# Kernel optimization log

Measured on AMD Instinct MI355X. Metric: run time of the kernel, lower is better.

## Reference

```python
import jax, jax.numpy as jnp
import numpy as np

B, T, N, D = 16, 24, 2048, 64
L, K = 2, 3  # num_layers, cheb_k


def setup_inputs() -> dict:
    key = jax.random.key(0)
    ks = jax.random.split(key, 6)
    x = jax.random.normal(ks[0], (B, T, N, D), dtype=jnp.float32)
    init_state = jnp.zeros((L, B, N, D), dtype=jnp.float32)
    adj = jax.random.uniform(ks[1], (N, N), dtype=jnp.float32)
    adj = adj / jnp.sum(adj, axis=-1, keepdims=True)  # row-normalized adjacency
    cin = 2 * D
    Wg = jax.random.normal(ks[2], (L, K, cin, 2 * D), dtype=jnp.float32) * (1.0 / np.sqrt(K * cin))
    bg = jnp.zeros((L, 2 * D), dtype=jnp.float32)
    Wu = jax.random.normal(ks[3], (L, K, cin, D), dtype=jnp.float32) * (1.0 / np.sqrt(K * cin))
    bu = jnp.zeros((L, D), dtype=jnp.float32)
    return {"x": x, "init_state": init_state, "adj_matrix": adj,
            "Wg": Wg, "bg": bg, "Wu": Wu, "bu": bu}


def _cheb_supports(adj, k):
    # T0=I, T1=A, Tk = 2*A@T_{k-1} - T_{k-2}
    n = adj.shape[0]
    sup = [jnp.eye(n, dtype=adj.dtype), adj]
    for _ in range(2, k):
        sup.append(2.0 * adj @ sup[-1] - sup[-2])
    return jnp.stack(sup[:k], axis=0)  # [K, N, N]


def _gconv(xs, supports, W, b):
    # xs: [B,N,Cin], supports: [K,N,N], W: [K,Cin,Cout]
    xg = jnp.einsum('knm,bmc->bknc', supports, xs)
    return jnp.einsum('bknc,kco->bno', xg, W) + b


def _cell(x_t, state, supports, Wg_l, bg_l, Wu_l, bu_l):
    ins = jnp.concatenate([x_t, state], axis=-1)  # [B,N,2D]
    zr = jax.nn.sigmoid(_gconv(ins, supports, Wg_l, bg_l))
    z, r = jnp.split(zr, 2, axis=-1)
    cand_in = jnp.concatenate([x_t, z * state], axis=-1)
    hc = jnp.tanh(_gconv(cand_in, supports, Wu_l, bu_l))
    return r * state + (1.0 - r) * hc


def reference(x, init_state, adj_matrix, Wg, bg, Wu, bu):
    supports = _cheb_supports(adj_matrix, K)
    current = x  # [B,T,N,D]
    hiddens = []
    for l in range(L):
        def step(state, x_t, l=l):
            new = _cell(x_t, state, supports, Wg[l], bg[l], Wu[l], bu[l])
            return new, new
        last, seq = jax.lax.scan(step, init_state[l], jnp.swapaxes(current, 0, 1))
        hiddens.append(last)
        current = x + jnp.swapaxes(seq, 0, 1)  # residual over the stacked states
    return current, jnp.stack(hiddens, axis=0)
```

## Files before the change

### kernel.cpp

```cpp
#include <hip/hip_runtime.h>
#include <hip/hip_bf16.h>
#include <math.h>

typedef __bf16 bf16x8 __attribute__((ext_vector_type(8)));
typedef float f32x4 __attribute__((ext_vector_type(4)));
typedef __hip_bfloat16 bf16s;

constexpr int kB = 16, kT = 24, kN = 2048, kD = 64;
constexpr size_t kBND = (size_t)kB * kN * kD;

struct Slot { const void* p0; const void* p1; int astr0, trow0, astr1, trow1, type; };
struct Slots6 { Slot s[6]; };
struct DiffGrp { const bf16s* src; bf16s* oA; bf16s* oA2; };
struct DiffP { const bf16s* S0; const bf16s* S1; DiffGrp g[4]; int colsPerGrp; };

__device__ __forceinline__ void async_copy16(void* lds, const void* g) {
  __builtin_amdgcn_global_load_lds((const __attribute__((address_space(1))) void*)g,
                                   (__attribute__((address_space(3))) void*)lds,
                                   16, 0, 0);
}


__device__ __forceinline__ void diff_core(
    const bf16s* __restrict__ S, const bf16s* __restrict__ Bsrc,
    int m0, int c0, bf16s* lA, bf16s* lB, f32x4 (&acc)[4][4])
{
  const int tid = threadIdx.x, lane = tid & 63, wave = tid >> 6;
  const int wm = (wave >> 1) * 64, wn = (wave & 1) * 64;
  const f32x4 zero = {0.f, 0.f, 0.f, 0.f};
#pragma unroll
  for (int i = 0; i < 4; ++i)
#pragma unroll
    for (int j = 0; j < 4; ++j) acc[i][j] = zero;

  const int ra = tid >> 3;
  const int cs = ((tid & 7) ^ (ra & 7)) * 8;
  const int rk0 = ((lane >> 4) ^ (lane & 7)) * 8;
  const int rk1 = ((4 + (lane >> 4)) ^ (lane & 7)) * 8;

  for (int k0 = 0; k0 < 2048; k0 += 64) {
#pragma unroll
    for (int i = 0; i < 4; ++i) {
      async_copy16(lA + (size_t)(i * 256 + tid) * 8,
                   S + (size_t)(m0 + i * 32 + ra) * 2048 + k0 + cs);
      async_copy16(lB + (size_t)(i * 256 + tid) * 8,
                   Bsrc + (size_t)(c0 + i * 32 + ra) * 2048 + k0 + cs);
    }
    __syncthreads();
#pragma unroll
    for (int ks = 0; ks < 2; ++ks) {
      const int rk = ks ? rk1 : rk0;
      bf16x8 av[4], bv[4];
#pragma unroll
      for (int f = 0; f < 4; ++f) {
        av[f] = *(const bf16x8*)(lA + (size_t)(wm + f * 16 + (lane & 15)) * 64 + rk);
        bv[f] = *(const bf16x8*)(lB + (size_t)(wn + f * 16 + (lane & 15)) * 64 + rk);
      }
#pragma unroll
      for (int i = 0; i < 4; ++i)
#pragma unroll
        for (int j = 0; j < 4; ++j)
          acc[i][j] = __builtin_amdgcn_mfma_f32_16x16x32_bf16(av[i], bv[j], acc[i][j], 0, 0, 0);
    }
    __syncthreads();
  }
}

__global__ __launch_bounds__(256) void k_diff(DiffP p)
{
  __shared__ bf16s lA[128 * 64];
  __shared__ bf16s lB[128 * 64];
  const int mi = blockIdx.x;
  const bf16s* S = (mi >> 4) ? p.S1 : p.S0;
  const int m0 = (mi & 15) * 128;
  const int ybpg = p.colsPerGrp >> 7;
  const int grp = blockIdx.y / ybpg;
  const int c0 = (blockIdx.y - grp * ybpg) * 128;
  const DiffGrp G = p.g[grp];

  f32x4 acc[4][4];
  diff_core(S, G.src, m0, c0, lA, lB, acc);

  bf16s* out = (mi >> 4) ? G.oA2 : G.oA;
  const int lane = threadIdx.x & 63, wave = threadIdx.x >> 6;
  const int wm = (wave >> 1) * 64, wn = (wave & 1) * 64;
  const int rq = (lane >> 4) * 4, cl = lane & 15;
#pragma unroll
  for (int fm = 0; fm < 4; ++fm)
#pragma unroll
    for (int fn = 0; fn < 4; ++fn)
#pragma unroll
      for (int q = 0; q < 4; ++q) {
        int gm = m0 + wm + fm * 16 + rq + q;
        int gc = c0 + wn + fn * 16 + cl;
        size_t off = ((size_t)(gc >> 6) * 2048 + gm) * 64 + (gc & 63);
        out[off] = __float2bfloat16(acc[fm][fn][q]);
      }
}

__global__ __launch_bounds__(256) void k_a2(
    const bf16s* __restrict__ A, const bf16s* __restrict__ AT, bf16s* A2)
{
  __shared__ bf16s lA[128 * 64];
  __shared__ bf16s lB[128 * 64];
  const int m0 = blockIdx.x * 128, n0 = blockIdx.y * 128;
  f32x4 acc[4][4];
  diff_core(A, AT, m0, n0, lA, lB, acc);
  const int lane = threadIdx.x & 63, wave = threadIdx.x >> 6;
  const int wm = (wave >> 1) * 64, wn = (wave & 1) * 64;
  const int rq = (lane >> 4) * 4, cl = lane & 15;
#pragma unroll
  for (int fm = 0; fm < 4; ++fm)
#pragma unroll
    for (int fn = 0; fn < 4; ++fn)
#pragma unroll
      for (int q = 0; q < 4; ++q) {
        int gm = m0 + wm + fm * 16 + rq + q;
        int gc = n0 + wn + fn * 16 + cl;
        A2[(size_t)gm * 2048 + gc] = __float2bfloat16(2.f * acc[fm][fn][q] - (gm == gc ? 1.f : 0.f));
      }
}

template<int BN>
__device__ __forceinline__ void small_core(
    const Slots6& sl, int m0, const bf16s* __restrict__ W,
    bf16s* lA, bf16s* lB, f32x4 (&acc)[4][BN / 32])
{
  const int tid = threadIdx.x, lane = tid & 63, wave = tid >> 6;
  const int wm = (wave >> 1) * 64, wn = (wave & 1) * (BN / 2);
  const f32x4 zero = {0.f, 0.f, 0.f, 0.f};
#pragma unroll
  for (int i = 0; i < 4; ++i)
#pragma unroll
    for (int j = 0; j < BN / 32; ++j) acc[i][j] = zero;

  const int ra = tid >> 3;
  const int cs = ((tid & 7) ^ (ra & 7)) * 8;
  const int rk0 = ((lane >> 4) ^ (lane & 7)) * 8;
  const int rk1 = ((4 + (lane >> 4)) ^ (lane & 7)) * 8;

#pragma unroll
  for (int ks = 0; ks < 6; ++ks) {
    const Slot sd = sl.s[ks];
    if (sd.type == 0) {
      const bf16s* base = (const bf16s*)sd.p0;
#pragma unroll
      for (int i = 0; i < 4; ++i) {
        int row = m0 + i * 32 + ra;
        size_t roff = ((size_t)(row >> 11) * sd.astr0 + sd.trow0 + (row & 2047)) * 64 + cs;
        async_copy16(lA + (size_t)(i * 256 + tid) * 8, base + roff);
      }
    } else if (sd.type == 1) {
#pragma unroll
      for (int i = 0; i < 4; ++i) {
        int row = m0 + i * 32 + ra;
        size_t roff = ((size_t)(row >> 11) * sd.astr0 + sd.trow0 + (row & 2047)) * 64 + cs;
        const float4* q0 = (const float4*)((const float*)sd.p0 + roff);
        float4 a = q0[0], b = q0[1];
        union { bf16x8 v; bf16s h[8]; } u;
        u.h[0] = __float2bfloat16(a.x); u.h[1] = __float2bfloat16(a.y);
        u.h[2] = __float2bfloat16(a.z); u.h[3] = __float2bfloat16(a.w);
        u.h[4] = __float2bfloat16(b.x); u.h[5] = __float2bfloat16(b.y);
        u.h[6] = __float2bfloat16(b.z); u.h[7] = __float2bfloat16(b.w);
        *(bf16x8*)(lA + (size_t)(i * 256 + tid) * 8) = u.v;
      }
    } else {
#pragma unroll
      for (int i = 0; i < 4; ++i) {
        int row = m0 + i * 32 + ra;
        size_t r0o = ((size_t)(row >> 11) * sd.astr0 + sd.trow0 + (row & 2047)) * 64 + cs;
        size_t r1o = ((size_t)(row >> 11) * sd.astr1 + sd.trow1 + (row & 2047)) * 64 + cs;
        union { bf16x8 v; bf16s h[8]; } a, b, o;
        a.v = *(const bf16x8*)((const bf16s*)sd.p0 + r0o);
        b.v = *(const bf16x8*)((const bf16s*)sd.p1 + r1o);
#pragma unroll
        for (int j = 0; j < 8; ++j)
          o.h[j] = __float2bfloat16(__bfloat162float(a.h[j]) + __bfloat162float(b.h[j]));
        *(bf16x8*)(lA + (size_t)(i * 256 + tid) * 8) = o.v;
      }
    }
#pragma unroll
    for (int i = 0; i < BN / 32; ++i)
      async_copy16(lB + (size_t)(i * 256 + tid) * 8,
                   W + (size_t)(i * 32 + ra) * 384 + ks * 64 + cs);
    __syncthreads();
#pragma unroll
    for (int kss = 0; kss < 2; ++kss) {
      const int rk = kss ? rk1 : rk0;
      bf16x8 av[4], bv[BN / 32];
#pragma unroll
      for (int f = 0; f < 4; ++f)
        av[f] = *(const bf16x8*)(lA + (size_t)(wm + f * 16 + (lane & 15)) * 64 + rk);
#pragma unroll
      for (int f = 0; f < BN / 32; ++f)
        bv[f] = *(const bf16x8*)(lB + (size_t)(wn + f * 16 + (lane & 15)) * 64 + rk);
#pragma unroll
      for (int i = 0; i < 4; ++i)
#pragma unroll
        for (int j = 0; j < BN / 32; ++j)
          acc[i][j] = __builtin_amdgcn_mfma_f32_16x16x32_bf16(av[i], bv[j], acc[i][j], 0, 0, 0);
    }
    __syncthreads();
  }
}

struct LayerG {
  Slots6 sl; const bf16s* W; const float* bias;
  const float* h; bf16s* zh; bf16s* zhT; float* r;
};
__global__ __launch_bounds__(256) void k_gate(LayerG A, LayerG B, int nA)
{
  __shared__ bf16s lA[128 * 64];
  __shared__ bf16s lB[128 * 64];
  const int bx = blockIdx.x;
  const bool isA = bx < nA;
  const LayerG L = isA ? A : B;
  const int m0 = (isA ? bx : bx - nA) * 128;
  f32x4 acc[4][4];
  small_core<128>(L.sl, m0, L.W, lA, lB, acc);
  const int lane = threadIdx.x & 63, wave = threadIdx.x >> 6;
  const int wm = (wave >> 1) * 64, wn = (wave & 1) * 64;
  const int rq = (lane >> 4) * 4, cl = lane & 15;
#pragma unroll
  for (int fm = 0; fm < 4; ++fm)
#pragma unroll
    for (int fn = 0; fn < 4; ++fn) {
      const int o = wn + fn * 16 + cl;
      const float bias = L.bias[o];
#pragma unroll
      for (int q = 0; q < 4; ++q) {
        size_t gm = (size_t)m0 + wm + fm * 16 + rq + q;
        float s = 1.f / (1.f + expf(-(acc[fm][fn][q] + bias)));
        if (o < 64) {
          float zh = s * L.h[gm * 64 + o];
          L.zh[gm * 64 + o] = __float2bfloat16(zh);
          L.zhT[((size_t)((gm >> 11) * 64 + o)) * 2048 + (gm & 2047)] = __float2bfloat16(zh);
        } else {
          L.r[gm * 64 + (o - 64)] = s;
        }
      }
    }
}

struct LayerC {
  Slots6 sl; const bf16s* W; const float* bias;
  const float* r; float* h32; bf16s* hT; bf16s* h_bf; float* hid;
  bf16s* x1;
  float* outC;
  const float* x0; int t;
};
__global__ __launch_bounds__(256) void k_cand(LayerC A, LayerC B, int nA)
{
  __shared__ bf16s lA[128 * 64];
  __shared__ bf16s lB[64 * 64];
  const int bx = blockIdx.x;
  const bool isA = bx < nA;
  const LayerC L = isA ? A : B;
  const int m0 = (isA ? bx : bx - nA) * 128;
  f32x4 acc[4][2];
  small_core<64>(L.sl, m0, L.W, lA, lB, acc);
  const int lane = threadIdx.x & 63, wave = threadIdx.x >> 6;
  const int wm = (wave >> 1) * 64, wn = (wave & 1) * 32;
  const int rq = (lane >> 4) * 4, cl = lane & 15;
#pragma unroll
  for (int fm = 0; fm < 4; ++fm)
#pragma unroll
    for (int fn = 0; fn < 2; ++fn) {
      const int d = wn + fn * 16 + cl;
      const float bias = L.bias[d];
#pragma unroll
      for (int q = 0; q < 4; ++q) {
        size_t gm = (size_t)m0 + wm + fm * 16 + rq + q;
        float hc = tanhf(acc[fm][fn][q] + bias);
        float r = L.r[gm * 64 + d];
        float h = L.h32[gm * 64 + d];
        float hn = r * h + (1.f - r) * hc;
        L.h32[gm * 64 + d] = hn;
        int b = (int)(gm >> 11), n = (int)(gm & 2047);
        L.hT[((size_t)(b * 64 + d)) * 2048 + n] = __float2bfloat16(hn);
        L.h_bf[gm * 64 + d] = __float2bfloat16(hn);
        size_t xi = (((size_t)b * kT + L.t) * 2048 + n) * 64 + d;
        if (L.x1) L.x1[gm * 64 + d] = __float2bfloat16(L.x0[xi] + hn);
        if (L.outC) L.outC[xi] = L.x0[xi] + hn;
        if (L.hid) L.hid[gm * 64 + d] = hn;
      }
    }
}

__global__ __launch_bounds__(256) void transpose_cvt(
    const float* in, bf16s* out, int nrows, int ncols,
    size_t in_ostride, size_t out_ostride)
{
  __shared__ float tile[64][65];
  const int r0 = blockIdx.x * 64, c0 = blockIdx.y * 64;
  in  += (size_t)blockIdx.z * in_ostride;
  out += (size_t)blockIdx.z * out_ostride;
  const int tx = threadIdx.x & 63, ty = threadIdx.x >> 6;
#pragma unroll
  for (int i = 0; i < 64; i += 4)
    tile[ty + i][tx] = in[(size_t)(r0 + ty + i) * ncols + c0 + tx];
  __syncthreads();
#pragma unroll
  for (int i = 0; i < 64; i += 4)
    out[(size_t)(c0 + ty + i) * nrows + r0 + tx] = __float2bfloat16(tile[tx][ty + i]);
}

__global__ __launch_bounds__(256) void k_cvt(const float* in, bf16s* out, int n)
{
  int i = blockIdx.x * 256 + threadIdx.x;
  if (i < n) out[i] = __float2bfloat16(in[i]);
}

__global__ __launch_bounds__(256) void k_repack(
    const float* Wg, const float* Wu, bf16s* WgT, bf16s* WuT)
{
  int idx = blockIdx.x * 256 + threadIdx.x;
  if (idx < 2 * 3 * 128 * 128) {
    int o = idx & 127, cin = (idx >> 7) & 127, k = (idx >> 14) % 3, l = idx / 49152;
    WgT[((size_t)(l * 128 + o)) * 384 + (2 * k + (cin >> 6)) * 64 + (cin & 63)] =
        __float2bfloat16(Wg[idx]);
  }
  if (idx < 2 * 3 * 128 * 64) {
    int o = idx & 63, cin = (idx >> 6) & 127, k = (idx >> 13) % 3, l = idx / 24576;
    WuT[((size_t)(l * 64 + o)) * 384 + (2 * k + (cin >> 6)) * 64 + (cin & 63)] =
        __float2bfloat16(Wu[idx]);
  }
}

__global__ __launch_bounds__(256) void init_layer(
    const float* ist_l, float* h32, bf16s* hT, bf16s* h_bf)
{
  size_t idx = (size_t)blockIdx.x * 256 + threadIdx.x;
  if (idx >= kBND) return;
  int d = (int)(idx & 63);
  size_t row = idx >> 6;
  int n = (int)(row & 2047), b = (int)(row >> 11);
  float h = ist_l[idx];
  h32[idx] = h;
  hT[((size_t)(b * 64 + d)) * 2048 + n] = __float2bfloat16(h);
  h_bf[idx] = __float2bfloat16(h);
}

extern "C" void kernel_launch(void* const* d_in, const int* in_sizes, int n_in,
                              void* d_out, int out_size, void* d_ws, size_t ws_size,
                              hipStream_t stream)
{
  (void)in_sizes; (void)n_in; (void)out_size; (void)ws_size;
  const float* x   = (const float*)d_in[0];
  const float* ist = (const float*)d_in[1];
  const float* adj = (const float*)d_in[2];
  const float* Wg  = (const float*)d_in[3];
  const float* bg  = (const float*)d_in[4];
  const float* Wu  = (const float*)d_in[5];
  const float* bu  = (const float*)d_in[6];
  float* outCur = (float*)d_out;
  float* outHid = outCur + (size_t)kB * kT * kN * kD;

  char* p = (char*)d_ws;
  auto carve = [&](size_t bytes) { char* q = p; p += (bytes + 255) & ~(size_t)255; return q; };
  bf16s* A_bf  = (bf16s*)carve((size_t)2048 * 2048 * 2);
  bf16s* A2_bf = (bf16s*)carve((size_t)2048 * 2048 * 2);
  bf16s* WgT   = (bf16s*)carve((size_t)2 * 128 * 384 * 2);
  bf16s* WuT   = (bf16s*)carve((size_t)2 * 64 * 384 * 2);
  float* h32b  = (float*)carve(2 * kBND * 4);
  float* r32b  = (float*)carve(2 * kBND * 4);
  bf16s* hTb   = (bf16s*)carve(2 * kBND * 2);
  bf16s* hbfb  = (bf16s*)carve(2 * kBND * 2);
  bf16s* zhTb  = (bf16s*)carve(2 * kBND * 2);
  bf16s* zhbfb = (bf16s*)carve(2 * kBND * 2);
  bf16s* x1b   = (bf16s*)carve(2 * kBND * 2);
  bf16s* sAh0  = (bf16s*)carve(kBND * 2);
  bf16s* sA2h0 = (bf16s*)carve(kBND * 2);
  bf16s* sAh1  = (bf16s*)carve(kBND * 2);
  bf16s* sA2h1 = (bf16s*)carve(kBND * 2);
  bf16s* sZ0   = (bf16s*)carve(kBND * 2);
  bf16s* sA2Z0 = (bf16s*)carve(kBND * 2);
  bf16s* sZ1   = (bf16s*)carve(kBND * 2);
  bf16s* sA2Z1 = (bf16s*)carve(kBND * 2);
  const size_t xTfull = (size_t)kB * kT * kD * kN * 2;
  bf16s* AxF  = (bf16s*)carve(xTfull);
  bf16s* A2xF = (bf16s*)carve(xTfull);
  bf16s* xTh  = (bf16s*)carve(xTfull / 2);
  bf16s* AT_bf = AxF;

  float* h32_0 = h32b;   float* h32_1 = h32b + kBND;
  float* r32_0 = r32b;   float* r32_1 = r32b + kBND;
  bf16s* hT0 = hTb;      bf16s* hT1 = hTb + kBND;
  bf16s* hbf0 = hbfb;    bf16s* hbf1 = hbfb + kBND;
  bf16s* zhT0 = zhTb;    bf16s* zhT1 = zhTb + kBND;
  bf16s* zhbf0 = zhbfb;  bf16s* zhbf1 = zhbfb + kBND;

  k_cvt<<<dim3((2048 * 2048 + 255) / 256), 256, 0, stream>>>(adj, A_bf, 2048 * 2048);
  transpose_cvt<<<dim3(32, 32, 1), 256, 0, stream>>>(adj, AT_bf, 2048, 2048, 0, 0);
  k_a2<<<dim3(16, 16, 1), 256, 0, stream>>>(A_bf, AT_bf, A2_bf);
  k_repack<<<dim3(384), 256, 0, stream>>>(Wg, Wu, WgT, WuT);
  init_layer<<<dim3((int)(kBND / 256)), 256, 0, stream>>>(ist, h32_0, hT0, hbf0);
  init_layer<<<dim3((int)(kBND / 256)), 256, 0, stream>>>(ist + kBND, h32_1, hT1, hbf1);

  for (int h = 0; h < 2; ++h) {
    size_t off = (size_t)h * 8 * kT * 131072;
    transpose_cvt<<<dim3(32, 1, 8 * kT), 256, 0, stream>>>(x + off, xTh, 2048, 64, 131072, 131072);
    DiffP dp; dp.S0 = A_bf; dp.S1 = A2_bf; dp.colsPerGrp = 12288;
    dp.g[0] = DiffGrp{xTh, AxF + off, A2xF + off};
    dp.g[1] = dp.g[2] = dp.g[3] = DiffGrp{nullptr, nullptr, nullptr};
    k_diff<<<dim3(32, 96), 256, 0, stream>>>(dp);
  }

  auto Sb = [](const void* p0, int astr, int trow) {
    return Slot{p0, nullptr, astr, trow, 0, 0, 0};
  };
  auto Sf = [](const void* p0, int astr, int trow) {
    return Slot{p0, nullptr, astr, trow, 0, 0, 1};
  };
  auto S2 = [](const void* p0, const void* p1, int astr1, int trow1) {
    return Slot{p0, p1, 2048, 0, astr1, trow1, 2};
  };

  for (int s = 0; s <= kT; ++s) {
    const bool aA = (s < kT), aB = (s >= 1);
    const int tA = s, tB = s - 1;
    const int nA = aA ? 256 : 0, nB = aB ? 256 : 0;
    bf16s* x1cur = x1b + (size_t)(s & 1) * kBND;
    bf16s* x1prev = x1b + (size_t)((s - 1) & 1) * kBND;

    {
      DiffP dp; dp.S0 = A_bf; dp.S1 = A2_bf; dp.colsPerGrp = 1024;
      int ng = 0;
      dp.g[ng++] = DiffGrp{hT0, sAh0, sA2h0};
      if (aB) dp.g[ng++] = DiffGrp{hT1, sAh1, sA2h1};
      for (int i = ng; i < 4; ++i) dp.g[i] = DiffGrp{nullptr, nullptr, nullptr};
      k_diff<<<dim3(32, 8 * ng), 256, 0, stream>>>(dp);
    }

    {
      LayerG GA = {}, GB = {};
      if (aA) {
        GA.sl.s[0] = Sf(x, kT * 2048, tA * 2048);
        GA.sl.s[1] = Sb(hbf0, 2048, 0);
        GA.sl.s[2] = Sb(AxF, kT * 2048, tA * 2048);
        GA.sl.s[3] = Sb(sAh0, 2048, 0);
        GA.sl.s[4] = Sb(A2xF, kT * 2048, tA * 2048);
        GA.sl.s[5] = Sb(sA2h0, 2048, 0);
        GA.W = WgT; GA.bias = bg; GA.h = h32_0; GA.zh = zhbf0; GA.zhT = zhT0; GA.r = r32_0;
      }
      if (aB) {
        GB.sl.s[0] = Sb(x1prev, 2048, 0);
        GB.sl.s[1] = Sb(hbf1, 2048, 0);
        GB.sl.s[2] = S2(sAh0, AxF, kT * 2048, tB * 2048);
        GB.sl.s[3] = Sb(sAh1, 2048, 0);
        GB.sl.s[4] = S2(sA2h0, A2xF, kT * 2048, tB * 2048);
        GB.sl.s[5] = Sb(sA2h1, 2048, 0);
        GB.W = WgT + (size_t)128 * 384; GB.bias = bg + 128;
        GB.h = h32_1; GB.zh = zhbf1; GB.zhT = zhT1; GB.r = r32_1;
      }
      k_gate<<<dim3(nA + nB), 256, 0, stream>>>(GA, GB, nA);
    }

    {
      DiffP dp; dp.S0 = A_bf; dp.S1 = A2_bf; dp.colsPerGrp = 1024;
      int ng = 0;
      if (aA) dp.g[ng++] = DiffGrp{zhT0, sZ0, sA2Z0};
      if (aB) dp.g[ng++] = DiffGrp{zhT1, sZ1, sA2Z1};
      for (int i = ng; i < 4; ++i) dp.g[i] = DiffGrp{nullptr, nullptr, nullptr};
      k_diff<<<dim3(32, 8 * ng), 256, 0, stream>>>(dp);
    }

    {
      LayerC CA = {}, CB = {};
      if (aA) {
        CA.sl.s[0] = Sf(x, kT * 2048, tA * 2048);
        CA.sl.s[1] = Sb(zhbf0, 2048, 0);
        CA.sl.s[2] = Sb(AxF, kT * 2048, tA * 2048);
        CA.sl.s[3] = Sb(sZ0, 2048, 0);
        CA.sl.s[4] = Sb(A2xF, kT * 2048, tA * 2048);
        CA.sl.s[5] = Sb(sA2Z0, 2048, 0);
        CA.W = WuT; CA.bias = bu; CA.r = r32_0; CA.h32 = h32_0; CA.hT = hT0; CA.h_bf = hbf0;
        CA.hid = (tA == kT - 1) ? outHid : nullptr;
        CA.x1 = x1cur; CA.outC = nullptr; CA.x0 = x; CA.t = tA;
      }
      if (aB) {
        CB.sl.s[0] = Sb(x1prev, 2048, 0);
        CB.sl.s[1] = Sb(zhbf1, 2048, 0);
        CB.sl.s[2] = S2(sAh0, AxF, kT * 2048, tB * 2048);
        CB.sl.s[3] = Sb(sZ1, 2048, 0);
        CB.sl.s[4] = S2(sA2h0, A2xF, kT * 2048, tB * 2048);
        CB.sl.s[5] = Sb(sA2Z1, 2048, 0);
        CB.W = WuT + (size_t)64 * 384; CB.bias = bu + 64;
        CB.r = r32_1; CB.h32 = h32_1; CB.hT = hT1; CB.h_bf = hbf1;
        CB.hid = (tB == kT - 1) ? outHid + kBND : nullptr;
        CB.x1 = nullptr; CB.outC = outCur; CB.x0 = x; CB.t = tB;
      }
      k_cand<<<dim3(nA + nB), 256, 0, stream>>>(CA, CB, nA);
    }
  }
}
```

Baseline: 5.091 ms.

## Fuse candidate-path diffusion of z*h into the candidate GEMM kernel

Replaces the separate k_diff launch for z*h and the k_cand launch with a single k_dcand kernel. Each block first computes A@zh and A2@zh for a 64-node by two-batch tile, sharing the zh tile between both supports. It writes the results to global memory, then runs the candidate GEMM and GRU update on exactly those rows. This removes one launch and one kernel boundary per timestep and improves locality of the diffusion outputs. In exchange, the diffusion and GEMM phases within a block run serially, and the kernel always launches 512 blocks, with inactive layers exiting early.

```diff
diff --git a/kernel.cpp b/kernel.cpp
--- a/kernel.cpp
+++ b/kernel.cpp
@@ -64,6 +64,28 @@
     }
     __syncthreads();
   }
+}
+
+__device__ __forceinline__ void diff_tile(
+    const bf16s* __restrict__ S, const bf16s* __restrict__ src, bf16s* out,
+    int m0, int c0, bf16s* lA, bf16s* lB)
+{
+  f32x4 acc[4][4];
+  diff_core(S, src, m0, c0, lA, lB, acc);
+  const int lane = threadIdx.x & 63, wave = threadIdx.x >> 6;
+  const int wm = (wave >> 1) * 64, wn = (wave & 1) * 64;
+  const int rq = (lane >> 4) * 4, cl = lane & 15;
+#pragma unroll
+  for (int fm = 0; fm < 4; ++fm)
+#pragma unroll
+    for (int fn = 0; fn < 4; ++fn)
+#pragma unroll
+      for (int q = 0; q < 4; ++q) {
+        int gm = m0 + wm + fm * 16 + rq + q;
+        int gc = c0 + wn + fn * 16 + cl;
+        size_t off = ((size_t)(gc >> 6) * 2048 + gm) * 64 + (gc & 63);
+        out[off] = __float2bfloat16(acc[fm][fn][q]);
+      }
 }
 
 __global__ __launch_bounds__(256) void k_diff(DiffP p)
@@ -77,25 +99,8 @@
   const int grp = blockIdx.y / ybpg;
   const int c0 = (blockIdx.y - grp * ybpg) * 128;
   const DiffGrp G = p.g[grp];
-
-  f32x4 acc[4][4];
-  diff_core(S, G.src, m0, c0, lA, lB, acc);
-
   bf16s* out = (mi >> 4) ? G.oA2 : G.oA;
-  const int lane = threadIdx.x & 63, wave = threadIdx.x >> 6;
-  const int wm = (wave >> 1) * 64, wn = (wave & 1) * 64;
-  const int rq = (lane >> 4) * 4, cl = lane & 15;
-#pragma unroll
-  for (int fm = 0; fm < 4; ++fm)
-#pragma unroll
-    for (int fn = 0; fn < 4; ++fn)
-#pragma unroll
-      for (int q = 0; q < 4; ++q) {
-        int gm = m0 + wm + fm * 16 + rq + q;
-        int gc = c0 + wn + fn * 16 + cl;
-        size_t off = ((size_t)(gc >> 6) * 2048 + gm) * 64 + (gc & 63);
-        out[off] = __float2bfloat16(acc[fm][fn][q]);
-      }
+  diff_tile(S, G.src, out, m0, c0, lA, lB);
 }
 
 __global__ __launch_bounds__(256) void k_a2(
@@ -242,47 +247,249 @@
     }
 }
 
-struct LayerC {
-  Slots6 sl; const bf16s* W; const float* bias;
-  const float* r; float* h32; bf16s* hT; bf16s* h_bf; float* hid;
-  bf16s* x1;
-  float* outC;
-  const float* x0; int t;
+__device__ __forceinline__ Slot Sb_d(const void* p0, int astr, int trow) {
+  return Slot{p0, nullptr, astr, trow, 0, 0, 0};
+}
+__device__ __forceinline__ Slot Sf_d(const void* p0, int astr, int trow) {
+  return Slot{p0, nullptr, astr, trow, 0, 0, 1};
+}
+__device__ __forceinline__ Slot S2_d(const void* p0, const void* p1, int astr1, int trow1) {
+  return Slot{p0, p1, 2048, 0, astr1, trow1, 2};
+}
+
+struct CandP {
+  const bf16s *A, *A2;
+  const bf16s *zhT0, *zhT1;
+  bf16s *sZ0, *sA2Z0, *sZ1, *sA2Z1;
+  const float *x;
+  const bf16s *zhbf0, *zhbf1, *x1prev;
+  const bf16s *AxF, *A2xF, *sAh0, *sA2h0;
+  const bf16s *WuT; const float *bu;
+  const float *r32_0, *r32_1;
+  float *h32_0, *h32_1;
+  bf16s *hT0, *hT1, *hbf0, *hbf1;
+  bf16s *x1cur;
+  float *outCur, *outHid;
+  int tA, tB, aA, aB;
 };
-__global__ __launch_bounds__(256) void k_cand(LayerC A, LayerC B, int nA)
-{
-  __shared__ bf16s lA[128 * 64];
-  __shared__ bf16s lB[64 * 64];
-  const int bx = blockIdx.x;
-  const bool isA = bx < nA;
-  const LayerC L = isA ? A : B;
-  const int m0 = (isA ? bx : bx - nA) * 128;
-  f32x4 acc[4][2];
-  small_core<64>(L.sl, m0, L.W, lA, lB, acc);
-  const int lane = threadIdx.x & 63, wave = threadIdx.x >> 6;
-  const int wm = (wave >> 1) * 64, wn = (wave & 1) * 32;
+
+__global__ __launch_bounds__(256, 2) void k_dcand(CandP P)
+{
+  __shared__ bf16s lds[16384];
+  const int layer = blockIdx.x >> 8;
+  if (layer ? !P.aB : !P.aA) return;
+  const int lin = blockIdx.x & 255;
+  const int mb = (lin & 7) | (((lin >> 6) & 3) << 3);
+  const int cb = (lin >> 3) & 7;
+  const int m0 = mb * 64, c0 = cb * 128, b0 = cb * 2;
+  const int t = layer ? P.tB : P.tA;
+
+  const int tid = threadIdx.x, lane = tid & 63, wave = tid >> 6;
+  const int ra = tid >> 3;
+  const int cs = ((tid & 7) ^ (ra & 7)) * 8;
+  const int rk0 = ((lane >> 4) ^ (lane & 7)) * 8;
+  const int rk1 = ((4 + (lane >> 4)) ^ (lane & 7)) * 8;
+
+  {
+    bf16s* lA  = lds;
+    bf16s* lA2 = lds + 4096;
+    bf16s* lB  = lds + 8192;
+    const int wm = (wave >> 1) * 32, wn = (wave & 1) * 64;
+    const bf16s* src = layer ? P.zhT1 : P.zhT0;
+
+    f32x4 acc[2][2][4];
+    const f32x4 zero = {0.f, 0.f, 0.f, 0.f};
+#pragma unroll
+    for (int s = 0; s < 2; ++s)
+#pragma unroll
+      for (int i = 0; i < 2; ++i)
+#pragma unroll
+        for (int j = 0; j < 4; ++j) acc[s][i][j] = zero;
+
+    for (int k0 = 0; k0 < 2048; k0 += 64) {
+#pragma unroll
+      for (int i = 0; i < 2; ++i) {
+        async_copy16(lA  + (size_t)(i * 256 + tid) * 8,
+                     P.A  + (size_t)(m0 + i * 32 + ra) * 2048 + k0 + cs);
+        async_copy16(lA2 + (size_t)(i * 256 + tid) * 8,
+                     P.A2 + (size_t)(m0 + i * 32 + ra) * 2048 + k0 + cs);
+      }
+#pragma unroll
+      for (int i = 0; i < 4; ++i)
+        async_copy16(lB + (size_t)(i * 256 + tid) * 8,
+                     src + (size_t)(c0 + i * 32 + ra) * 2048 + k0 + cs);
+      __syncthreads();
+#pragma unroll
+      for (int ks = 0; ks < 2; ++ks) {
+        const int rk = ks ? rk1 : rk0;
+        bf16x8 av0[2], av1[2], bv[4];
+#pragma unroll
+        for (int f = 0; f < 2; ++f) {
+          av0[f] = *(const bf16x8*)(lA  + (size_t)(wm + f * 16 + (lane & 15)) * 64 + rk);
+          av1[f] = *(const bf16x8*)(lA2 + (size_t)(wm + f * 16 + (lane & 15)) * 64 + rk);
+        }
+#pragma unroll
+        for (int f = 0; f < 4; ++f)
+          bv[f] = *(const bf16x8*)(lB + (size_t)(wn + f * 16 + (lane & 15)) * 64 + rk);
+#pragma unroll
+        for (int i = 0; i < 2; ++i)
+#pragma unroll
+          for (int j = 0; j < 4; ++j) {
+            acc[0][i][j] = __builtin_amdgcn_mfma_f32_16x16x32_bf16(av0[i], bv[j], acc[0][i][j], 0, 0, 0);
+            acc[1][i][j] = __builtin_amdgcn_mfma_f32_16x16x32_bf16(av1[i], bv[j], acc[1][i][j], 0, 0, 0);
+          }
+      }
+      __syncthreads();
+    }
+
+    bf16s* oZ0 = layer ? P.sZ1   : P.sZ0;
+    bf16s* oZ1 = layer ? P.sA2Z1 : P.sA2Z0;
+    const int rq = (lane >> 4) * 4, cl = lane & 15;
+#pragma unroll
+    for (int sp = 0; sp < 2; ++sp) {
+      bf16s* out = sp ? oZ1 : oZ0;
+#pragma unroll
+      for (int fm = 0; fm < 2; ++fm)
+#pragma unroll
+        for (int fn = 0; fn < 4; ++fn)
+#pragma unroll
+          for (int q = 0; q < 4; ++q) {
+            int gm = m0 + wm + fm * 16 + rq + q;
+            int gc = c0 + wn + fn * 16 + cl;
+            out[((size_t)(gc >> 6) * 2048 + gm) * 64 + (gc & 63)] =
+                __float2bfloat16(acc[sp][fm][fn][q]);
+          }
+    }
+  }
+  __syncthreads();
+
+  Slots6 sl;
+  if (!layer) {
+    sl.s[0] = Sf_d(P.x, kT * 2048, P.tA * 2048);
+    sl.s[1] = Sb_d(P.zhbf0, 2048, 0);
+    sl.s[2] = Sb_d(P.AxF, kT * 2048, P.tA * 2048);
+    sl.s[3] = Sb_d(P.sZ0, 2048, 0);
+    sl.s[4] = Sb_d(P.A2xF, kT * 2048, P.tA * 2048);
+    sl.s[5] = Sb_d(P.sA2Z0, 2048, 0);
+  } else {
+    sl.s[0] = Sb_d(P.x1prev, 2048, 0);
+    sl.s[1] = Sb_d(P.zhbf1, 2048, 0);
+    sl.s[2] = S2_d(P.sAh0, P.AxF, kT * 2048, P.tB * 2048);
+    sl.s[3] = Sb_d(P.sZ1, 2048, 0);
+    sl.s[4] = S2_d(P.sA2h0, P.A2xF, kT * 2048, P.tB * 2048);
+    sl.s[5] = Sb_d(P.sA2Z1, 2048, 0);
+  }
+  const bf16s* W = P.WuT + (size_t)layer * 64 * 384;
+  const float* bias = P.bu + layer * 64;
+
+  bf16s* gA = lds;
+  bf16s* gB = lds + 8192;
+  const int wmG = (wave >> 1) * 64, wnG = (wave & 1) * 32;
+  f32x4 gacc[4][2];
+  const f32x4 zero = {0.f, 0.f, 0.f, 0.f};
+#pragma unroll
+  for (int i = 0; i < 4; ++i)
+#pragma unroll
+    for (int j = 0; j < 2; ++j) gacc[i][j] = zero;
+
+#pragma unroll
+  for (int ks = 0; ks < 6; ++ks) {
+    const Slot sd = sl.s[ks];
+    if (sd.type == 0) {
+      const bf16s* base = (const bf16s*)sd.p0;
+#pragma unroll
+      for (int i = 0; i < 4; ++i) {
+        int vrow = i * 32 + ra;
+        size_t gm = (size_t)(b0 + (vrow >> 6)) * 2048 + m0 + (vrow & 63);
+        size_t roff = ((gm >> 11) * sd.astr0 + sd.trow0 + (gm & 2047)) * 64 + cs;
+        async_copy16(gA + (size_t)(i * 256 + tid) * 8, base + roff);
+      }
+    } else if (sd.type == 1) {
+#pragma unroll
+      for (int i = 0; i < 4; ++i) {
+        int vrow = i * 32 + ra;
+        size_t gm = (size_t)(b0 + (vrow >> 6)) * 2048 + m0 + (vrow & 63);
+        size_t roff = ((gm >> 11) * sd.astr0 + sd.trow0 + (gm & 2047)) * 64 + cs;
+        const float4* q0 = (const float4*)((const float*)sd.p0 + roff);
+        float4 a = q0[0], b = q0[1];
+        union { bf16x8 v; bf16s h[8]; } u;
+        u.h[0] = __float2bfloat16(a.x); u.h[1] = __float2bfloat16(a.y);
+        u.h[2] = __float2bfloat16(a.z); u.h[3] = __float2bfloat16(a.w);
+        u.h[4] = __float2bfloat16(b.x); u.h[5] = __float2bfloat16(b.y);
+        u.h[6] = __float2bfloat16(b.z); u.h[7] = __float2bfloat16(b.w);
+        *(bf16x8*)(gA + (size_t)(i * 256 + tid) * 8) = u.v;
+      }
+    } else {
+#pragma unroll
+      for (int i = 0; i < 4; ++i) {
+        int vrow = i * 32 + ra;
+        size_t gm = (size_t)(b0 + (vrow >> 6)) * 2048 + m0 + (vrow & 63);
+        size_t r0o = ((gm >> 11) * sd.astr0 + sd.trow0 + (gm & 2047)) * 64 + cs;
+        size_t r1o = ((gm >> 11) * sd.astr1 + sd.trow1 + (gm & 2047)) * 64 + cs;
+        union { bf16x8 v; bf16s h[8]; } a, b, o;
+        a.v = *(const bf16x8*)((const bf16s*)sd.p0 + r0o);
+        b.v = *(const bf16x8*)((const bf16s*)sd.p1 + r1o);
+#pragma unroll
+        for (int j = 0; j < 8; ++j)
+          o.h[j] = __float2bfloat16(__bfloat162float(a.h[j]) + __bfloat162float(b.h[j]));
+        *(bf16x8*)(gA + (size_t)(i * 256 + tid) * 8) = o.v;
+      }
+    }
+#pragma unroll
+    for (int i = 0; i < 2; ++i)
+      async_copy16(gB + (size_t)(i * 256 + tid) * 8,
+                   W + (size_t)(i * 32 + ra) * 384 + ks * 64 + cs);
+    __syncthreads();
+#pragma unroll
+    for (int kss = 0; kss < 2; ++kss) {
+      const int rk = kss ? rk1 : rk0;
+      bf16x8 av[4], bv[2];
+#pragma unroll
+      for (int f = 0; f < 4; ++f)
+        av[f] = *(const bf16x8*)(gA + (size_t)(wmG + f * 16 + (lane & 15)) * 64 + rk);
+#pragma unroll
+      for (int f = 0; f < 2; ++f)
+        bv[f] = *(const bf16x8*)(gB + (size_t)(wnG + f * 16 + (lane & 15)) * 64 + rk);
+#pragma unroll
+      for (int i = 0; i < 4; ++i)
+#pragma unroll
+        for (int j = 0; j < 2; ++j)
+          gacc[i][j] = __builtin_amdgcn_mfma_f32_16x16x32_bf16(av[i], bv[j], gacc[i][j], 0, 0, 0);
+    }
+    __syncthreads();
+  }
+
+  const float* r32 = layer ? P.r32_1 : P.r32_0;
+  float* h32 = layer ? P.h32_1 : P.h32_0;
+  bf16s* hT  = layer ? P.hT1  : P.hT0;
+  bf16s* hbf = layer ? P.hbf1 : P.hbf0;
   const int rq = (lane >> 4) * 4, cl = lane & 15;
 #pragma unroll
   for (int fm = 0; fm < 4; ++fm)
 #pragma unroll
     for (int fn = 0; fn < 2; ++fn) {
-      const int d = wn + fn * 16 + cl;
-      const float bias = L.bias[d];
+      const int d = wnG + fn * 16 + cl;
+      const float bias_d = bias[d];
 #pragma unroll
       for (int q = 0; q < 4; ++q) {
-        size_t gm = (size_t)m0 + wm + fm * 16 + rq + q;
-        float hc = tanhf(acc[fm][fn][q] + bias);
-        float r = L.r[gm * 64 + d];
-        float h = L.h32[gm * 64 + d];
+        int vrow = wmG + fm * 16 + rq + q;
+        size_t gm = (size_t)(b0 + (vrow >> 6)) * 2048 + m0 + (vrow & 63);
+        float hc = tanhf(gacc[fm][fn][q] + bias_d);
+        float r = r32[gm * 64 + d];
+        float h = h32[gm * 64 + d];
         float hn = r * h + (1.f - r) * hc;
-        L.h32[gm * 64 + d] = hn;
+        h32[gm * 64 + d] = hn;
         int b = (int)(gm >> 11), n = (int)(gm & 2047);
-        L.hT[((size_t)(b * 64 + d)) * 2048 + n] = __float2bfloat16(hn);
-        L.h_bf[gm * 64 + d] = __float2bfloat16(hn);
-        size_t xi = (((size_t)b * kT + L.t) * 2048 + n) * 64 + d;
-        if (L.x1) L.x1[gm * 64 + d] = __float2bfloat16(L.x0[xi] + hn);
-        if (L.outC) L.outC[xi] = L.x0[xi] + hn;
-        if (L.hid) L.hid[gm * 64 + d] = hn;
+        hT[((size_t)(b * 64 + d)) * 2048 + n] = __float2bfloat16(hn);
+        hbf[gm * 64 + d] = __float2bfloat16(hn);
+        size_t xi = (((size_t)b * kT + t) * 2048 + n) * 64 + d;
+        if (!layer) {
+          P.x1cur[gm * 64 + d] = __float2bfloat16(P.x[xi] + hn);
+          if (t == kT - 1) P.outHid[gm * 64 + d] = hn;
+        } else {
+          P.outCur[xi] = P.x[xi] + hn;
+          if (t == kT - 1) (P.outHid + kBND)[gm * 64 + d] = hn;
+        }
       }
     }
 }
@@ -406,12 +613,8 @@
     k_diff<<<dim3(32, 96), 256, 0, stream>>>(dp);
   }
 
-  auto Sb = [](const void* p0, int astr, int trow) {
-    return Slot{p0, nullptr, astr, trow, 0, 0, 0};
-  };
-  auto Sf = [](const void* p0, int astr, int trow) {
-    return Slot{p0, nullptr, astr, trow, 0, 0, 1};
-  };
+  auto Sb = [](const void* p0, int astr, int trow) { return Slot{p0, nullptr, astr, trow, 0, 0, 0}; };
+  auto Sf = [](const void* p0, int astr, int trow) { return Slot{p0, nullptr, astr, trow, 0, 0, 1}; };
   auto S2 = [](const void* p0, const void* p1, int astr1, int trow1) {
     return Slot{p0, p1, 2048, 0, astr1, trow1, 2};
   };
@@ -420,7 +623,7 @@
     const bool aA = (s < kT), aB = (s >= 1);
     const int tA = s, tB = s - 1;
     const int nA = aA ? 256 : 0, nB = aB ? 256 : 0;
-    bf16s* x1cur = x1b + (size_t)(s & 1) * kBND;
+    bf16s* x1cur  = x1b + (size_t)(s & 1) * kBND;
     bf16s* x1prev = x1b + (size_t)((s - 1) & 1) * kBND;
 
     {
@@ -457,40 +660,19 @@
     }
 
     {
-      DiffP dp; dp.S0 = A_bf; dp.S1 = A2_bf; dp.colsPerGrp = 1024;
-      int ng = 0;
-      if (aA) dp.g[ng++] = DiffGrp{zhT0, sZ0, sA2Z0};
-      if (aB) dp.g[ng++] = DiffGrp{zhT1, sZ1, sA2Z1};
-      for (int i = ng; i < 4; ++i) dp.g[i] = DiffGrp{nullptr, nullptr, nullptr};
-      k_diff<<<dim3(32, 8 * ng), 256, 0, stream>>>(dp);
-    }
-
-    {
-      LayerC CA = {}, CB = {};
-      if (aA) {
-        CA.sl.s[0] = Sf(x, kT * 2048, tA * 2048);
-        CA.sl.s[1] = Sb(zhbf0, 2048, 0);
-        CA.sl.s[2] = Sb(AxF, kT * 2048, tA * 2048);
-        CA.sl.s[3] = Sb(sZ0, 2048, 0);
-        CA.sl.s[4] = Sb(A2xF, kT * 2048, tA * 2048);
-        CA.sl.s[5] = Sb(sA2Z0, 2048, 0);
-        CA.W = WuT; CA.bias = bu; CA.r = r32_0; CA.h32 = h32_0; CA.hT = hT0; CA.h_bf = hbf0;
-        CA.hid = (tA == kT - 1) ? outHid : nullptr;
-        CA.x1 = x1cur; CA.outC = nullptr; CA.x0 = x; CA.t = tA;
-      }
-      if (aB) {
-        CB.sl.s[0] = Sb(x1prev, 2048, 0);
-        CB.sl.s[1] = Sb(zhbf1, 2048, 0);
-        CB.sl.s[2] = S2(sAh0, AxF, kT * 2048, tB * 2048);
-        CB.sl.s[3] = Sb(sZ1, 2048, 0);
-        CB.sl.s[4] = S2(sA2h0, A2xF, kT * 2048, tB * 2048);
-        CB.sl.s[5] = Sb(sA2Z1, 2048, 0);
-        CB.W = WuT + (size_t)64 * 384; CB.bias = bu + 64;
-        CB.r = r32_1; CB.h32 = h32_1; CB.hT = hT1; CB.h_bf = hbf1;
-        CB.hid = (tB == kT - 1) ? outHid + kBND : nullptr;
-        CB.x1 = nullptr; CB.outC = outCur; CB.x0 = x; CB.t = tB;
-      }
-      k_cand<<<dim3(nA + nB), 256, 0, stream>>>(CA, CB, nA);
-    }
-  }
-}
+      CandP P;
+      P.A = A_bf; P.A2 = A2_bf;
+      P.zhT0 = zhT0; P.zhT1 = zhT1;
+      P.sZ0 = sZ0; P.sA2Z0 = sA2Z0; P.sZ1 = sZ1; P.sA2Z1 = sA2Z1;
+      P.x = x; P.zhbf0 = zhbf0; P.zhbf1 = zhbf1; P.x1prev = x1prev;
+      P.AxF = AxF; P.A2xF = A2xF; P.sAh0 = sAh0; P.sA2h0 = sA2h0;
+      P.WuT = WuT; P.bu = bu;
+      P.r32_0 = r32_0; P.r32_1 = r32_1;
+      P.h32_0 = h32_0; P.h32_1 = h32_1;
+      P.hT0 = hT0; P.hT1 = hT1; P.hbf0 = hbf0; P.hbf1 = hbf1;
+      P.x1cur = x1cur; P.outCur = outCur; P.outHid = outHid;
+      P.tA = tA; P.tB = tB; P.aA = aA ? 1 : 0; P.aB = aB ? 1 : 0;
+      k_dcand<<<dim3(512), 256, 0, stream>>>(P);
+    }
+  }
+}
```

New measurement: 4.764 ms. 6.4% less time.
